# Kernel tuning notes

Measured on AMD Instinct MI355X. Metric: run time of the kernel, lower is better.

The kernel has to match this reference:

```python
import jax, jax.numpy as jnp
import numpy as np

N, P, Q, H_DIM, HEADS, D = 4096, 128, 128, 256, 8, 64  # D = graph_dim // heads


def setup_inputs() -> dict:
    key = jax.random.key(0)
    ks = jax.random.split(key, 6)
    s = 0.05  # small scale to keep tanh/softmax in a sane range
    return {
        "x_prices": jax.random.normal(ks[0], (N, P), jnp.float32),
        "x_news": jax.random.normal(ks[1], (N, Q), jnp.float32),
        "W_bil": jax.random.normal(ks[2], (H_DIM, P, Q), jnp.float32) * s,
        "b_bil": jax.random.normal(ks[3], (H_DIM,), jnp.float32) * s,
        "Wt": jax.random.normal(ks[4], (HEADS, D, H_DIM), jnp.float32) * s,
        "a_vec": jax.random.normal(ks[5], (HEADS, 2 * D), jnp.float32) * s,
    }


def reference(x_prices, x_news, W_bil, b_bil, Wt, a_vec):
    # nn.Bilinear: out[n,h] = sum_pq x_prices[n,p] W[h,p,q] x_news[n,q] + b[h]
    x = jnp.einsum('np,hpq,nq->nh', x_prices, W_bil, x_news) + b_bil  # (N, hidden)

    # Per-head linear transform: fc_transform (no bias). Wt: (heads, d, hidden)
    xt = jnp.einsum('nh,kdh->knd', x, Wt)  # (heads, N, d)

    # Attention score a . [x_i, x_j] split into src/dst halves -> broadcast add
    d = Wt.shape[1]
    a_src, a_dst = a_vec[:, :d], a_vec[:, d:]
    s_src = jnp.einsum('knd,kd->kn', xt, a_src)  # (heads, N)
    s_dst = jnp.einsum('knd,kd->kn', xt, a_dst)  # (heads, N)
    scores = s_src[:, :, None] + s_dst[:, None, :]  # (heads, N, N)
    scores = jnp.where(scores >= 0, scores, 0.2 * scores)  # LeakyReLU(0.2)

    attn = jax.nn.softmax(scores, axis=-1)  # softmax over neighbors j
    out = jnp.einsum('knm,kmd->knd', attn, xt)  # (heads, N, d)

    # Concatenate head outputs on feature dim, then tanh
    out = jnp.transpose(out, (1, 0, 2)).reshape(xt.shape[1], -1)  # (N, heads*d)
    return jnp.tanh(out)
```

## Files before the change

### kernel.cpp

```cpp
#include <hip/hip_runtime.h>
#include <hip/hip_bf16.h>

typedef unsigned short ushort;
typedef unsigned int uint;
typedef unsigned long long u64;
typedef _Float16 f16;

#define NN 4096
#define PP 128
#define QQ 128
#define HD 256
#define KH 8
#define DD 64
#define KK 16384

typedef _Float16 f16x2 __attribute__((ext_vector_type(2)));
typedef _Float16 f16x4 __attribute__((ext_vector_type(4)));
typedef _Float16 f16x8 __attribute__((ext_vector_type(8)));
typedef __fp16 fp16x2 __attribute__((ext_vector_type(2)));
typedef float f32x4 __attribute__((ext_vector_type(4)));

__device__ inline void async_lds16(const void* g, void* l) {
  __builtin_amdgcn_global_load_lds(
      (const __attribute__((address_space(1))) unsigned int*)g,
      (__attribute__((address_space(3))) unsigned int*)l, 16, 0, 0);
}

__global__ __launch_bounds__(256) void k0_split2(
    const float* __restrict__ W, const float* __restrict__ Wt,
    f16* __restrict__ hiW, f16* __restrict__ loW,
    f16* __restrict__ hiT, f16* __restrict__ loT, float* __restrict__ xz) {
  const int tid = blockIdx.x * 256 + threadIdx.x;
  const int i = tid * 4;
  if (tid < (NN * HD) / 4)
    *(float4*)&xz[i] = make_float4(0.f, 0.f, 0.f, 0.f);
  const float* src;
  f16 *hi, *lo;
  int off;
  if (i < HD * PP * QQ) { src = W; hi = hiW; lo = loW; off = i; }
  else { src = Wt; hi = hiT; lo = loT; off = i - HD * PP * QQ; }
  const float4 w = *(const float4*)&src[off];
  const float wf[4] = {w.x, w.y, w.z, w.w};
  f16x4 hv, lv;
#pragma unroll
  for (int j = 0; j < 4; ++j) {
    const f16 h = (f16)wf[j];
    hv[j] = h;
    lv[j] = (f16)(wf[j] - (float)h);
  }
  *(f16x4*)&hi[off] = hv;
  *(f16x4*)&lo[off] = lv;
}

__global__ __launch_bounds__(256, 4) void k1_bilinear(
    const float* __restrict__ xp, const float* __restrict__ xn,
    const f16* __restrict__ Whi, const f16* __restrict__ Wlo,
    float* __restrict__ xout) {
  __shared__ f16 whi[128 * 32];
  __shared__ f16 wlo[128 * 32];
  __shared__ f16 zhi[128 * 40];
  __shared__ float xpt[8][128];

  const int t = threadIdx.x;
  const int n0 = blockIdx.x * 128;
  const int kb = blockIdx.y * (KK / 16);
  const int h0 = blockIdx.z * 128;
  const int pb = kb >> 7;

  for (int idx = t; idx < 1024; idx += 256) {
    const int p = idx & 7, n = idx >> 3;
    xpt[p][n] = xp[(size_t)(n0 + n) * PP + pb + p];
  }

  const int l = t & 63, w = t >> 6;
  const int wr = (w >> 1) * 64, wc = (w & 1) * 64;

  int aoff[4], boff[4];
#pragma unroll
  for (int i = 0; i < 4; ++i)
    aoff[i] = (wr + i * 16 + (l & 15)) * 40 + (l >> 4) * 8;
#pragma unroll
  for (int j = 0; j < 4; ++j) {
    const int hr = wc + j * 16 + (l & 15);
    boff[j] = hr * 32 + (((l >> 4) ^ ((hr ^ (hr >> 2)) & 3)) * 8);
  }

  const int shb = t >> 2, seg = t & 3;
  int gsw[2];
#pragma unroll
  for (int g = 0; g < 2; ++g) {
    const int r = shb + 64 * g;
    gsw[g] = seg ^ ((r ^ (r >> 2)) & 3);
  }

  const int zn = t >> 1, zko = (t & 1) * 16;

  f32x4 acc[4][4];
#pragma unroll
  for (int i = 0; i < 4; ++i)
#pragma unroll
    for (int j = 0; j < 4; ++j) acc[i][j] = (f32x4)0.f;

  for (int c = 0; c < 32; ++c) {
    const int kc = kb + c * 32;
    const int pl = c >> 2;
    const int q0 = (c & 3) * 32;

    __syncthreads();

#pragma unroll
    for (int g = 0; g < 2; ++g) {
      const int r = shb + 64 * g;
      async_lds16(Whi + (size_t)(h0 + r) * KK + kc + gsw[g] * 8,
                  whi + r * 32 + seg * 8);
      async_lds16(Wlo + (size_t)(h0 + r) * KK + kc + gsw[g] * 8,
                  wlo + r * 32 + seg * 8);
    }

    {
      const float xpv = xpt[pl][zn];
      const float* xr = xn + (size_t)(n0 + zn) * QQ + q0 + zko;
      const float4 v0 = ((const float4*)xr)[0];
      const float4 v1 = ((const float4*)xr)[1];
      const float4 v2 = ((const float4*)xr)[2];
      const float4 v3 = ((const float4*)xr)[3];
      float zz[16] = {v0.x, v0.y, v0.z, v0.w, v1.x, v1.y, v1.z, v1.w,
                      v2.x, v2.y, v2.z, v2.w, v3.x, v3.y, v3.z, v3.w};
      union { uint u[8]; uint4 q[2]; } ph;
#pragma unroll
      for (int j = 0; j < 8; ++j) {
        union { fp16x2 h; uint u; } cv;
        cv.h = __builtin_amdgcn_cvt_pkrtz(xpv * zz[2 * j], xpv * zz[2 * j + 1]);
        ph.u[j] = cv.u;
      }
      const int zo = zn * 40 + zko;
      *(uint4*)&zhi[zo] = ph.q[0];
      *(uint4*)&zhi[zo + 8] = ph.q[1];
    }

    __syncthreads();

    f16x8 Ah[4];
#pragma unroll
    for (int i = 0; i < 4; ++i) Ah[i] = *(const f16x8*)&zhi[aoff[i]];
#pragma unroll
    for (int j = 0; j < 4; ++j) {
      const f16x8 Bh = *(const f16x8*)&whi[boff[j]];
      const f16x8 Bl = *(const f16x8*)&wlo[boff[j]];
#pragma unroll
      for (int i = 0; i < 4; ++i)
        acc[i][j] = __builtin_amdgcn_mfma_f32_16x16x32_f16(Ah[i], Bh, acc[i][j], 0, 0, 0);
#pragma unroll
      for (int i = 0; i < 4; ++i)
        acc[i][j] = __builtin_amdgcn_mfma_f32_16x16x32_f16(Ah[i], Bl, acc[i][j], 0, 0, 0);
    }
  }

#pragma unroll
  for (int i = 0; i < 4; ++i)
#pragma unroll
    for (int j = 0; j < 4; ++j) {
      const int row = n0 + wr + i * 16 + (l >> 4) * 4;
      const int col = h0 + wc + j * 16 + (l & 15);
#pragma unroll
      for (int r = 0; r < 4; ++r)
        atomicAdd(&xout[(size_t)(row + r) * HD + col], acc[i][j][r]);
    }
}

__global__ __launch_bounds__(256) void k23_xt(
    const float* __restrict__ x, const float* __restrict__ bb,
    const f16* __restrict__ Wthi, const f16* __restrict__ Wtlo,
    const float* __restrict__ av, float* __restrict__ xt,
    float* __restrict__ ssrc, float* __restrict__ sdst) {
  __shared__ f16 ah[64 * 40];
  __shared__ f16 bh[128 * 32];
  __shared__ f16 bl[128 * 32];
  __shared__ float red1[2][64][17];
  __shared__ float red2[2][64][17];
  const int t = threadIdx.x;
  const int n0 = blockIdx.x * 64;
  const int c0 = blockIdx.y * 128;
  const int l = t & 63, w = t >> 6;
  const int wn = (w & 1) * 32, wcc = (w >> 1) * 64;

  int aoff[2], boff[4];
#pragma unroll
  for (int i = 0; i < 2; ++i)
    aoff[i] = (wn + i * 16 + (l & 15)) * 40 + (l >> 4) * 8;
#pragma unroll
  for (int j = 0; j < 4; ++j) {
    const int hr = wcc + j * 16 + (l & 15);
    boff[j] = hr * 32 + (((l >> 4) ^ ((hr ^ (hr >> 2)) & 3)) * 8);
  }

  f32x4 acc[2][4];
#pragma unroll
  for (int i = 0; i < 2; ++i)
#pragma unroll
    for (int j = 0; j < 4; ++j) acc[i][j] = (f32x4)0.f;

  for (int kc = 0; kc < HD; kc += 32) {
    __syncthreads();
    {
      const int row = t >> 2, sg = t & 3;
      const float* xr = &x[(size_t)(n0 + row) * HD + kc + sg * 8];
      const float4 xa = ((const float4*)xr)[0];
      const float4 xb = ((const float4*)xr)[1];
      const float4 ba = *(const float4*)&bb[kc + sg * 8];
      const float4 bv = *(const float4*)&bb[kc + sg * 8 + 4];
      f16x8 o;
      o[0] = (f16)(xa.x + ba.x); o[1] = (f16)(xa.y + ba.y);
      o[2] = (f16)(xa.z + ba.z); o[3] = (f16)(xa.w + ba.w);
      o[4] = (f16)(xb.x + bv.x); o[5] = (f16)(xb.y + bv.y);
      o[6] = (f16)(xb.z + bv.z); o[7] = (f16)(xb.w + bv.w);
      *(f16x8*)&ah[row * 40 + sg * 8] = o;
    }
#pragma unroll
    for (int g = 0; g < 2; ++g) {
      const int slot = g * 256 + t;
      const int col = slot >> 2, ps = slot & 3;
      const int ls = ps ^ ((col ^ (col >> 2)) & 3);
      *(uint4*)&bh[col * 32 + ps * 8] =
          *(const uint4*)&Wthi[(size_t)(c0 + col) * HD + kc + ls * 8];
      *(uint4*)&bl[col * 32 + ps * 8] =
          *(const uint4*)&Wtlo[(size_t)(c0 + col) * HD + kc + ls * 8];
    }
    __syncthreads();
    f16x8 Af[2];
#pragma unroll
    for (int i = 0; i < 2; ++i) Af[i] = *(const f16x8*)&ah[aoff[i]];
#pragma unroll
    for (int j = 0; j < 4; ++j) {
      const f16x8 Bh = *(const f16x8*)&bh[boff[j]];
      const f16x8 Bl = *(const f16x8*)&bl[boff[j]];
#pragma unroll
      for (int i = 0; i < 2; ++i)
        acc[i][j] = __builtin_amdgcn_mfma_f32_16x16x32_f16(Af[i], Bh, acc[i][j], 0, 0, 0);
#pragma unroll
      for (int i = 0; i < 2; ++i)
        acc[i][j] = __builtin_amdgcn_mfma_f32_16x16x32_f16(Af[i], Bl, acc[i][j], 0, 0, 0);
    }
  }

  const int hh = w >> 1;
  const int khead = (c0 >> 6) + hh;
  float a1v[4], a2v[4];
#pragma unroll
  for (int j = 0; j < 4; ++j) {
    const int d = j * 16 + (l & 15);
    a1v[j] = av[khead * (2 * DD) + d];
    a2v[j] = av[khead * (2 * DD) + DD + d];
  }

#pragma unroll
  for (int i = 0; i < 2; ++i)
#pragma unroll
    for (int r = 0; r < 4; ++r) {
      const int rowl = wn + i * 16 + (l >> 4) * 4 + r;
      float p1 = 0.f, p2 = 0.f;
#pragma unroll
      for (int j = 0; j < 4; ++j) {
        p1 += acc[i][j][r] * a1v[j];
        p2 += acc[i][j][r] * a2v[j];
      }
      red1[hh][rowl][l & 15] = p1;
      red2[hh][rowl][l & 15] = p2;
    }

#pragma unroll
  for (int i = 0; i < 2; ++i)
#pragma unroll
    for (int j = 0; j < 4; ++j) {
      const int row = n0 + wn + i * 16 + (l >> 4) * 4;
      const int colg = c0 + wcc + j * 16 + (l & 15);
      const int k = colg >> 6, d = colg & 63;
#pragma unroll
      for (int r = 0; r < 4; ++r)
        xt[((size_t)(k * NN + row + r)) * DD + d] = acc[i][j][r];
    }

  __syncthreads();
  {
    const int hh2 = t >> 7;
    const int which = (t >> 6) & 1;
    const int row = t & 63;
    const float* rp = which ? &red2[hh2][row][0] : &red1[hh2][row][0];
    float s = 0.f;
#pragma unroll
    for (int g = 0; g < 16; ++g) s += rp[g];
    const int kk = (c0 >> 6) + hh2;
    if (which) sdst[kk * NN + n0 + row] = s;
    else ssrc[kk * NN + n0 + row] = s;
  }
}

__global__ __launch_bounds__(256) void k4_rank(
    const float* __restrict__ sdst, float* __restrict__ vsorted,
    int* __restrict__ perm) {
  __shared__ u64 kv[4096];
  const int k = blockIdx.y, t = threadIdx.x;
  for (int i = t; i < 4096; i += 256) {
    const uint u = __float_as_uint(sdst[k * NN + i]);
    const uint key = (u & 0x80000000u) ? ~u : (u | 0x80000000u);
    kv[i] = ((u64)key << 32) | (uint)i;
  }
  __syncthreads();
  const int m = blockIdx.x * 256 + t;
  const u64 my = kv[m];
  int cnt = 0;
#pragma unroll 16
  for (int j = 0; j < 4096; ++j) cnt += (kv[j] < my) ? 1 : 0;
  const uint key = (uint)(my >> 32);
  const uint u = (key & 0x80000000u) ? (key ^ 0x80000000u) : ~key;
  vsorted[k * NN + cnt] = __uint_as_float(u);
  perm[k * NN + cnt] = (int)(my & 0xFFFFFFFFu);
}

__global__ __launch_bounds__(64) void k4b_chunksum(
    const float* __restrict__ vs, const int* __restrict__ perm,
    const float* __restrict__ xt, float* __restrict__ Chi, float* __restrict__ Clo) {
  __shared__ float rows[64][64];
  __shared__ float eh[64], el[64];
  const int c = blockIdx.x, k = blockIdx.y, t = threadIdx.x;
  const int base = k * NN + c * 64;
  {
    const float v = vs[base + t];
    eh[t] = __expf(v);
    el[t] = __expf(0.2f * v);
  }
#pragma unroll
  for (int r = 0; r < 16; ++r) {
    const int i = r * 4 + (t >> 4);
    const int p = perm[base + i];
    *(float4*)&rows[i][(t & 15) * 4] =
        *(const float4*)&xt[((size_t)(k * NN + p)) * DD + (t & 15) * 4];
  }
  __syncthreads();
  float shi = 0.f, slo = 0.f, whs = 0.f, wls = 0.f;
#pragma unroll 8
  for (int i = 0; i < 64; ++i) {
    const float val = rows[i][t];
    shi += eh[i] * val; slo += el[i] * val;
    whs += eh[i]; wls += el[i];
  }
  const int cb = (k * 64 + c) * 65;
  Chi[cb + t] = shi;
  Clo[cb + t] = slo;
  if (t == 0) { Chi[cb + 64] = whs; Clo[cb + 64] = wls; }
}

__global__ __launch_bounds__(64) void k4d_expand(
    const float* __restrict__ vs, const int* __restrict__ perm,
    const float* __restrict__ xt, const float* __restrict__ Chi,
    const float* __restrict__ Clo, float* __restrict__ Phi,
    float* __restrict__ Plo) {
  __shared__ float schi[64 * 65];
  __shared__ float sclo[64 * 65];
  __shared__ float rows[64][64];
  __shared__ float eh[64], el[64];
  const int c = blockIdx.x, k = blockIdx.y, t = threadIdx.x;
  const int base = k * NN + c * 64;
  for (int idx = t; idx < 4160; idx += 64) {
    schi[idx] = Chi[k * 4160 + idx];
    sclo[idx] = Clo[k * 4160 + idx];
  }
  {
    const float v = vs[base + t];
    eh[t] = __expf(v);
    el[t] = __expf(0.2f * v);
  }
#pragma unroll
  for (int r = 0; r < 16; ++r) {
    const int i = r * 4 + (t >> 4);
    const int p = perm[base + i];
    *(float4*)&rows[i][(t & 15) * 4] =
        *(const float4*)&xt[((size_t)(k * NN + p)) * DD + (t & 15) * 4];
  }
  __syncthreads();

  float run = 0.f, wrun = 0.f;
  for (int cc = 0; cc < c; ++cc) {
    run += sclo[cc * 65 + t];
    wrun += sclo[cc * 65 + 64];
  }
  float runS = 0.f, wrunS = 0.f;
  for (int cc = c + 1; cc < 64; ++cc) {
    runS += schi[cc * 65 + t];
    wrunS += schi[cc * 65 + 64];
  }

  for (int i = 0; i < 64; ++i) {
    const size_t rb = ((size_t)(k * 4097) + c * 64 + i) * 65;
    Plo[rb + t] = run;
    if (t == 0) Plo[rb + 64] = wrun;
    run += el[i] * rows[i][t];
    wrun += el[i];
  }
  if (c == 63) {
    const size_t rb = ((size_t)(k * 4097) + 4096) * 65;
    Plo[rb + t] = run;
    if (t == 0) Plo[rb + 64] = wrun;
  }
  for (int i = 63; i >= 0; --i) {
    runS += eh[i] * rows[i][t];
    wrunS += eh[i];
    const size_t rb = ((size_t)(k * 4097) + c * 64 + i) * 65;
    Phi[rb + t] = runS;
    if (t == 0) Phi[rb + 64] = wrunS;
  }
  if (c == 63) {
    const size_t rb = ((size_t)(k * 4097) + 4096) * 65;
    Phi[rb + t] = 0.f;
    if (t == 0) Phi[rb + 64] = 0.f;
  }
}

__global__ __launch_bounds__(256) void k6_final(
    const float* __restrict__ ssrc, const float* __restrict__ vsorted,
    const float* __restrict__ Phi, const float* __restrict__ Plo,
    float* __restrict__ out) {
  __shared__ float vsh[4096];
  __shared__ int posSh[16];
  const int t = threadIdx.x;
  const int q0 = blockIdx.x * 16;
  const int k = q0 >> 12;
  for (int idx = t; idx < 1024; idx += 256)
    *(float4*)&vsh[idx * 4] = *(const float4*)&vsorted[k * NN + idx * 4];
  __syncthreads();
  if (t < 16) {
    const float thr = -ssrc[q0 + t];
    int lo = 0, hi = 4096;
    while (lo < hi) {
      const int mid = (lo + hi) >> 1;
      if (vsh[mid] < thr) lo = mid + 1; else hi = mid;
    }
    posSh[t] = lo;
  }
  __syncthreads();
  const int d = t & 63;
#pragma unroll
  for (int qq = 0; qq < 4; ++qq) {
    const int ql = qq * 4 + (t >> 6);
    const int qi = q0 + ql;
    const int n = qi & 4095;
    const float u = ssrc[qi];
    const size_t rb = ((size_t)(k * 4097) + posSh[ql]) * 65;
    const float eu = __expf(u), el = __expf(0.2f * u);
    const float num = eu * Phi[rb + d] + el * Plo[rb + d];
    const float den = eu * Phi[rb + 64] + el * Plo[rb + 64];
    out[(size_t)n * (KH * DD) + k * DD + d] = tanhf(num / den);
  }
}

extern "C" void kernel_launch(void* const* d_in, const int* in_sizes, int n_in,
                              void* d_out, int out_size, void* d_ws, size_t ws_size,
                              hipStream_t stream) {
  const float* xp = (const float*)d_in[0];
  const float* xn = (const float*)d_in[1];
  const float* W = (const float*)d_in[2];
  const float* bb = (const float*)d_in[3];
  const float* Wt = (const float*)d_in[4];
  const float* av = (const float*)d_in[5];
  float* out = (float*)d_out;

  char* ws = (char*)d_ws;
  f16* Whi    = (f16*)(ws);
  f16* Wlo    = (f16*)(ws + 8388608);
  float* Phi  = (float*)(ws);
  float* Plo  = (float*)(ws + 8522240);
  float* x    = (float*)(ws + 17044480);
  float* xt   = (float*)(ws + 21238784);
  f16* Wthi   = (f16*)(ws + 31724544);
  f16* Wtlo   = (f16*)(ws + 31986688);
  float* ssrc = (float*)(ws + 32248832);
  float* sdst = (float*)(ws + 32379904);
  float* vsort= (float*)(ws + 32510976);
  int*   perm = (int*)  (ws + 32642048);
  float* Chi  = (float*)(ws + 32773120);
  float* Clo  = (float*)(ws + 32906240);

  k0_split2<<<(HD * PP * QQ + KH * DD * HD) / 1024, 256, 0, stream>>>(
      W, Wt, Whi, Wlo, Wthi, Wtlo, x);
  k1_bilinear<<<dim3(NN / 128, 16, 2), 256, 0, stream>>>(xp, xn, Whi, Wlo, x);
  k23_xt<<<dim3(NN / 64, 4), 256, 0, stream>>>(x, bb, Wthi, Wtlo, av, xt, ssrc, sdst);
  k4_rank<<<dim3(16, KH), 256, 0, stream>>>(sdst, vsort, perm);
  k4b_chunksum<<<dim3(64, KH), 64, 0, stream>>>(vsort, perm, xt, Chi, Clo);
  k4d_expand<<<dim3(64, KH), 64, 0, stream>>>(vsort, perm, xt, Chi, Clo, Phi, Plo);
  k6_final<<<(KH * NN) / 16, 256, 0, stream>>>(ssrc, vsort, Phi, Plo, out);
}
```

Before: 280.0 us.

## Double-buffer bilinear weight tiles in LDS with async prefetch of next chunk

The bilinear kernel now keeps two LDS buffers for the hi/lo weight tiles. It issues async global-to-LDS loads for the next K-chunk while the current chunk's MFMAs run, and uses explicit s_waitcnt vmcnt counts with raw barriers instead of __syncthreads. The xn loads are also hoisted ahead of the prefetch. This adds LDS per block and lowers the launch-bounds occupancy hint from 4 to 3, and it relies on hand-counted vmcnt values being correct.

Result: slower. 286.8 us (+2.4%).

```diff
diff --git a/kernel.cpp b/kernel.cpp
--- a/kernel.cpp
+++ b/kernel.cpp
@@ -52,12 +52,12 @@
   *(f16x4*)&lo[off] = lv;
 }
 
-__global__ __launch_bounds__(256, 4) void k1_bilinear(
+__global__ __launch_bounds__(256, 3) void k1_bilinear(
     const float* __restrict__ xp, const float* __restrict__ xn,
     const f16* __restrict__ Whi, const f16* __restrict__ Wlo,
     float* __restrict__ xout) {
-  __shared__ f16 whi[128 * 32];
-  __shared__ f16 wlo[128 * 32];
+  __shared__ f16 whi[2][128 * 32];
+  __shared__ f16 wlo[2][128 * 32];
   __shared__ f16 zhi[128 * 40];
   __shared__ float xpt[8][128];
 
@@ -67,31 +67,44 @@
   const int h0 = blockIdx.z * 128;
   const int pb = kb >> 7;
 
+  const int l = t & 63, w = t >> 6;
+  const int wr = (w >> 1) * 64, wc = (w & 1) * 64;
+
+  int aoff[4], boff[4];
+#pragma unroll
+  for (int i = 0; i < 4; ++i)
+    aoff[i] = (wr + i * 16 + (l & 15)) * 40 + (l >> 4) * 8;
+#pragma unroll
+  for (int j = 0; j < 4; ++j) {
+    const int hr = wc + j * 16 + (l & 15);
+    boff[j] = hr * 32 + (((l >> 4) ^ ((hr ^ (hr >> 2)) & 3)) * 8);
+  }
+
+  const int shb = t >> 2, seg = t & 3;
+  int gsw[2];
+#pragma unroll
+  for (int g = 0; g < 2; ++g) {
+    const int r = shb + 64 * g;
+    gsw[g] = seg ^ ((r ^ (r >> 2)) & 3);
+  }
+
   for (int idx = t; idx < 1024; idx += 256) {
     const int p = idx & 7, n = idx >> 3;
     xpt[p][n] = xp[(size_t)(n0 + n) * PP + pb + p];
   }
 
-  const int l = t & 63, w = t >> 6;
-  const int wr = (w >> 1) * 64, wc = (w & 1) * 64;
-
-  int aoff[4], boff[4];
-#pragma unroll
-  for (int i = 0; i < 4; ++i)
-    aoff[i] = (wr + i * 16 + (l & 15)) * 40 + (l >> 4) * 8;
-#pragma unroll
-  for (int j = 0; j < 4; ++j) {
-    const int hr = wc + j * 16 + (l & 15);
-    boff[j] = hr * 32 + (((l >> 4) ^ ((hr ^ (hr >> 2)) & 3)) * 8);
-  }
-
-  const int shb = t >> 2, seg = t & 3;
-  int gsw[2];
-#pragma unroll
-  for (int g = 0; g < 2; ++g) {
-    const int r = shb + 64 * g;
-    gsw[g] = seg ^ ((r ^ (r >> 2)) & 3);
-  }
+  auto stage_w = [&](int buf, int kc_) {
+#pragma unroll
+    for (int g = 0; g < 2; ++g) {
+      const int r = shb + 64 * g;
+      async_lds16(Whi + (size_t)(h0 + r) * KK + kc_ + gsw[g] * 8,
+                  &whi[buf][r * 32 + seg * 8]);
+      async_lds16(Wlo + (size_t)(h0 + r) * KK + kc_ + gsw[g] * 8,
+                  &wlo[buf][r * 32 + seg * 8]);
+    }
+  };
+
+  stage_w(0, kb);
 
   const int zn = t >> 1, zko = (t & 1) * 16;
 
@@ -105,25 +118,22 @@
     const int kc = kb + c * 32;
     const int pl = c >> 2;
     const int q0 = (c & 3) * 32;
-
-    __syncthreads();
-
-#pragma unroll
-    for (int g = 0; g < 2; ++g) {
-      const int r = shb + 64 * g;
-      async_lds16(Whi + (size_t)(h0 + r) * KK + kc + gsw[g] * 8,
-                  whi + r * 32 + seg * 8);
-      async_lds16(Wlo + (size_t)(h0 + r) * KK + kc + gsw[g] * 8,
-                  wlo + r * 32 + seg * 8);
-    }
+    const int cur = c & 1, nxt = cur ^ 1;
+
+    asm volatile("s_waitcnt lgkmcnt(0)" ::: "memory");
+    __builtin_amdgcn_s_barrier();
+
+    const float* xr = xn + (size_t)(n0 + zn) * QQ + q0 + zko;
+    const float4 v0 = ((const float4*)xr)[0];
+    const float4 v1 = ((const float4*)xr)[1];
+    const float4 v2 = ((const float4*)xr)[2];
+    const float4 v3 = ((const float4*)xr)[3];
+    __builtin_amdgcn_sched_barrier(0);
+
+    if (c < 31) stage_w(nxt, kc + 32);
 
     {
       const float xpv = xpt[pl][zn];
-      const float* xr = xn + (size_t)(n0 + zn) * QQ + q0 + zko;
-      const float4 v0 = ((const float4*)xr)[0];
-      const float4 v1 = ((const float4*)xr)[1];
-      const float4 v2 = ((const float4*)xr)[2];
-      const float4 v3 = ((const float4*)xr)[3];
       float zz[16] = {v0.x, v0.y, v0.z, v0.w, v1.x, v1.y, v1.z, v1.w,
                       v2.x, v2.y, v2.z, v2.w, v3.x, v3.y, v3.z, v3.w};
       union { uint u[8]; uint4 q[2]; } ph;
@@ -138,15 +148,19 @@
       *(uint4*)&zhi[zo + 8] = ph.q[1];
     }
 
-    __syncthreads();
+    if (c < 31)
+      asm volatile("s_waitcnt vmcnt(4) lgkmcnt(0)" ::: "memory");
+    else
+      asm volatile("s_waitcnt vmcnt(0) lgkmcnt(0)" ::: "memory");
+    __builtin_amdgcn_s_barrier();
 
     f16x8 Ah[4];
 #pragma unroll
     for (int i = 0; i < 4; ++i) Ah[i] = *(const f16x8*)&zhi[aoff[i]];
 #pragma unroll
     for (int j = 0; j < 4; ++j) {
-      const f16x8 Bh = *(const f16x8*)&whi[boff[j]];
-      const f16x8 Bl = *(const f16x8*)&wlo[boff[j]];
+      const f16x8 Bh = *(const f16x8*)&whi[cur][boff[j]];
+      const f16x8 Bl = *(const f16x8*)&wlo[cur][boff[j]];
 #pragma unroll
       for (int i = 0; i < 4; ++i)
         acc[i][j] = __builtin_amdgcn_mfma_f32_16x16x32_f16(Ah[i], Bh, acc[i][j], 0, 0, 0);
```
